# Kernel tuning notes

Measured on AMD Instinct MI355X. Metric: run time of the kernel, lower is better.

## Reference

```python
import jax, jax.numpy as jnp
import numpy as np

EMB = 1024
HEADS = 16
HEAD_DIM = EMB // HEADS


def setup_inputs() -> dict:
    key = jax.random.key(0)
    ks = jax.random.split(key, 9)
    s = 1.0 / np.sqrt(EMB)
    x = jax.random.normal(ks[0], (2, 2048, EMB), dtype=jnp.float32)
    Wq = jax.random.normal(ks[1], (EMB, EMB), dtype=jnp.float32) * s
    bq = jnp.zeros((EMB,), dtype=jnp.float32)
    Wk = jax.random.normal(ks[2], (EMB, EMB), dtype=jnp.float32) * s
    bk = jnp.zeros((EMB,), dtype=jnp.float32)
    Wv = jax.random.normal(ks[3], (EMB, EMB), dtype=jnp.float32) * s
    bv = jnp.zeros((EMB,), dtype=jnp.float32)
    Wo = jax.random.normal(ks[4], (EMB, EMB), dtype=jnp.float32) * s
    bo = jnp.zeros((EMB,), dtype=jnp.float32)
    return {"x": x, "Wq": Wq, "bq": bq, "Wk": Wk, "bk": bk,
            "Wv": Wv, "bv": bv, "Wo": Wo, "bo": bo}


def reference(x, Wq, bq, Wk, bk, Wv, bv, Wo, bo):
    B, S, E = x.shape
    # torch Linear: y = x @ W.T + b
    q = x @ Wq.T + bq
    k = x @ Wk.T + bk
    v = x @ Wv.T + bv
    # [B,S,E] -> [B,H,S,D]
    q = q.reshape(B, S, HEADS, HEAD_DIM).transpose(0, 2, 1, 3)
    k = k.reshape(B, S, HEADS, HEAD_DIM).transpose(0, 2, 1, 3)
    v = v.reshape(B, S, HEADS, HEAD_DIM).transpose(0, 2, 1, 3)
    energy = jnp.einsum('bhqd,bhkd->bhqk', q, k)
    scaling = jnp.float32(E) ** 0.5  # NOTE: sqrt(emb_size), not sqrt(head_dim), as in source
    att = jax.nn.softmax(energy / scaling, axis=-1)
    out = jnp.einsum('bhqk,bhkd->bhqd', att, v)
    out = out.transpose(0, 2, 1, 3).reshape(B, S, E)
    return out @ Wo.T + bo
```

## Files before the change

kernel.cpp:

```cpp
#include <hip/hip_runtime.h>
#include <stdint.h>


typedef _Float16 half8  __attribute__((ext_vector_type(8)));
typedef _Float16 half4v __attribute__((ext_vector_type(4)));
typedef _Float16 half2v __attribute__((ext_vector_type(2)));
typedef float    f32x4  __attribute__((ext_vector_type(4)));

#define GLD16(g, l) __builtin_amdgcn_global_load_lds(                         \
    (__attribute__((address_space(1))) void*)(g),                            \
    (__attribute__((address_space(3))) void*)(l), 16, 0, 0)

#define MFMA16(a, b, c) __builtin_amdgcn_mfma_f32_16x16x32_f16((a), (b), (c), 0, 0, 0)

#if __has_builtin(__builtin_amdgcn_exp2f)
#define EXP2(x) __builtin_amdgcn_exp2f(x)
#else
#define EXP2(x) exp2f(x)
#endif

static __device__ inline half2v pk_f16(float a, float b)
{
#if __has_builtin(__builtin_amdgcn_cvt_pkrtz)
    auto t = __builtin_amdgcn_cvt_pkrtz(a, b);
    return *(half2v*)&t;
#else
    half2v r = { (_Float16)a, (_Float16)b };
    return r;
#endif
}

__global__ void cvt_all(const float* __restrict__ x,  const float* __restrict__ wq,
                        const float* __restrict__ wk, const float* __restrict__ wv,
                        const float* __restrict__ wo, _Float16* __restrict__ xb,
                        _Float16* __restrict__ wqkv, _Float16* __restrict__ wob)
{
    int i = blockIdx.x * blockDim.x + threadIdx.x;
    const float* src; _Float16* dst; int off;
    if (i < 1048576)      { src = x;  dst = xb;                 off = i; }
    else if (i < 1310720) { src = wq; dst = wqkv;               off = i - 1048576; }
    else if (i < 1572864) { src = wk; dst = wqkv + 1048576;     off = i - 1310720; }
    else if (i < 1835008) { src = wv; dst = wqkv + 2097152;     off = i - 1572864; }
    else                  { src = wo; dst = wob;                off = i - 1835008; }
    float4 f = ((const float4*)src)[off];
    half4v h = { (_Float16)f.x, (_Float16)f.y, (_Float16)f.z, (_Float16)f.w };
    ((half4v*)dst)[off] = h;
}

template<int BN, int MODE>
__global__ __launch_bounds__(256, MODE == 0 ? 3 : 2)
void gemm_f16(const _Float16* __restrict__ A, const _Float16* __restrict__ W,
              const float* __restrict__ b0, const float* __restrict__ b1,
              const float* __restrict__ b2, _Float16* __restrict__ o0,
              _Float16* __restrict__ o1, _Float16* __restrict__ o2,
              float* __restrict__ outf, float qscale)
{
    constexpr int NI = BN / 32;
    __shared__ _Float16 lA[128 * 64];
    __shared__ _Float16 lB[BN * 64];
    const int m0 = blockIdx.y * 128, n0 = blockIdx.x * BN;
    const int tid = threadIdx.x, lane = tid & 63, w = tid >> 6;
    const int wr = (w >> 1) * 64, wc = (w & 1) * (BN / 2);
    const int lrow = lane & 15, lk4 = lane >> 4;
    f32x4 acc[4][NI] = {};

    for (int k0 = 0; k0 < 1024; k0 += 64) {
        __syncthreads();
#pragma unroll
        for (int c = 0; c < 4; ++c) {
            int sidx = c * 256 + tid;
            int row = sidx >> 3, sl = sidx & 7;
            int gc = k0 + ((sl ^ (row & 7)) << 3);
            GLD16(A + (size_t)(m0 + row) * 1024 + gc, lA + (size_t)(c * 256 + w * 64) * 8);
        }
#pragma unroll
        for (int c = 0; c < BN / 32; ++c) {
            int sidx = c * 256 + tid;
            int row = sidx >> 3, sl = sidx & 7;
            int gc = k0 + ((sl ^ (row & 7)) << 3);
            GLD16(W + (size_t)(n0 + row) * 1024 + gc, lB + (size_t)(c * 256 + w * 64) * 8);
        }
        __syncthreads();

#pragma unroll
        for (int kd = 0; kd < 2; ++kd) {
            half8 af[4], bf[NI];
#pragma unroll
            for (int mi = 0; mi < 4; ++mi) {
                int ra = wr + mi * 16 + lrow;
                af[mi] = *(const half8*)(lA + ra * 64 + (((kd * 4 + lk4) ^ (ra & 7)) * 8));
            }
#pragma unroll
            for (int ni = 0; ni < NI; ++ni) {
                int rb = wc + ni * 16 + lrow;
                bf[ni] = *(const half8*)(lB + rb * 64 + (((kd * 4 + lk4) ^ (rb & 7)) * 8));
            }
#pragma unroll
            for (int mi = 0; mi < 4; ++mi)
#pragma unroll
                for (int ni = 0; ni < NI; ++ni)
                    acc[mi][ni] = MFMA16(af[mi], bf[ni], acc[mi][ni]);
        }
    }

    if (MODE == 0) {
        const int which = n0 >> 10;
        const float* bp = which == 0 ? b0 : which == 1 ? b1 : b2;
        _Float16* outh  = which == 0 ? o0 : which == 1 ? o1 : o2;
        const float scale = which == 0 ? qscale : 1.f;
        const int nh = n0 & 1023;
        float bcol[NI];
#pragma unroll
        for (int ni = 0; ni < NI; ++ni) bcol[ni] = bp[nh + wc + ni * 16 + lrow];
#pragma unroll
        for (int mi = 0; mi < 4; ++mi)
#pragma unroll
            for (int ni = 0; ni < NI; ++ni)
#pragma unroll
                for (int r = 0; r < 4; ++r) {
                    int rg = m0 + wr + mi * 16 + lk4 * 4 + r;
                    int cg = nh + wc + ni * 16 + lrow;
                    float v = (acc[mi][ni][r] + bcol[ni]) * scale;
                    int b = rg >> 11, s = rg & 2047, h = cg >> 6, d = cg & 63;
                    outh[(((size_t)b * 16 + h) * 2048 + s) * 64 + d] = (_Float16)v;
                }
    } else {
        float bcol[NI];
#pragma unroll
        for (int ni = 0; ni < NI; ++ni) bcol[ni] = b0[n0 + wc + ni * 16 + lrow];
#pragma unroll
        for (int mi = 0; mi < 4; ++mi)
#pragma unroll
            for (int ni = 0; ni < NI; ++ni)
#pragma unroll
                for (int r = 0; r < 4; ++r) {
                    int rg = m0 + wr + mi * 16 + lk4 * 4 + r;
                    int cg = n0 + wc + ni * 16 + lrow;
                    outf[(size_t)rg * 1024 + cg] = acc[mi][ni][r] + bcol[ni];
                }
    }
}

__global__ __launch_bounds__(256)
void transpose_v(const _Float16* __restrict__ v, _Float16* __restrict__ vt)
{
    __shared__ _Float16 t[64][68];
    const int bh = blockIdx.y, s0 = blockIdx.x * 64;
    const _Float16* vh = v + (size_t)bh * 2048 * 64;
    _Float16* vth = vt + (size_t)bh * 64 * 2048;
    const int tid = threadIdx.x;
#pragma unroll
    for (int j = 0; j < 2; ++j) {
        int ch = j * 256 + tid, r = ch >> 3, c = (ch & 7) * 8;
        half8 d = *(const half8*)(vh + (size_t)(s0 + r) * 64 + c);
#pragma unroll
        for (int i = 0; i < 8; ++i) t[r][c + i] = d[i];
    }
    __syncthreads();
#pragma unroll
    for (int j = 0; j < 2; ++j) {
        int ch = j * 256 + tid, d = ch >> 3, sc = (ch & 7) * 8;
        half8 o;
#pragma unroll
        for (int i = 0; i < 8; ++i) o[i] = t[sc + i][d];
        *(half8*)(vth + (size_t)d * 2048 + s0 + sc) = o;
    }
}

#define KVB 64
#define NT  32
__global__ __launch_bounds__(256, 3)
void attn(const _Float16* __restrict__ q, const _Float16* __restrict__ k,
          const _Float16* __restrict__ vt, _Float16* __restrict__ ao)
{
    __shared__ _Float16 lK[2][KVB * 64];
    __shared__ _Float16 lV[2][64 * KVB];
    __shared__ _Float16 lP[4][32 * KVB];
    const int bid0 = blockIdx.x;
    const int bid = (bid0 & 7) * 64 + (bid0 >> 3);
    const int bh = bid >> 4, q0 = (bid & 15) * 128;
    const int b = bh >> 4, h = bh & 15;
    const int tid = threadIdx.x, lane = tid & 63, w = tid >> 6;
    const int lrow = lane & 15, lk4 = lane >> 4;
    const _Float16* qh = q + (size_t)bh * 2048 * 64;
    const _Float16* kh = k + (size_t)bh * 2048 * 64;
    const _Float16* vth = vt + (size_t)bh * 64 * 2048;

    half8 qf[2][2];
#pragma unroll
    for (int ni = 0; ni < 2; ++ni)
#pragma unroll
        for (int kd = 0; kd < 2; ++kd)
            qf[ni][kd] = *(const half8*)(qh + (size_t)(q0 + w * 32 + ni * 16 + lrow) * 64
                                            + kd * 32 + lk4 * 8);

    float l_[2] = { 0.f, 0.f };
    f32x4 o[2][4] = {};

    auto STAGE = [&](int t, int bs) {
        const int s0 = t * KVB;
#pragma unroll
        for (int c = 0; c < 2; ++c) {
            int sidx = c * 256 + tid;
            int row = sidx >> 3, sl = sidx & 7;
            GLD16(kh + (size_t)(s0 + row) * 64 + ((sl ^ (row & 7)) * 8),
                  lK[bs] + (size_t)(c * 256 + w * 64) * 8);
            GLD16(vth + (size_t)row * 2048 + s0 + ((sl ^ (row & 7)) * 8),
                  lV[bs] + (size_t)(c * 256 + w * 64) * 8);
        }
    };

    STAGE(0, 0);
    STAGE(1, 1);

#pragma unroll 2
    for (int t = 0; t < NT; ++t) {
        const int cur = t & 1;
        if (t < NT - 1) asm volatile("s_waitcnt vmcnt(4)" ::: "memory");
        else            asm volatile("s_waitcnt vmcnt(0)" ::: "memory");
        __builtin_amdgcn_s_barrier();
        __builtin_amdgcn_sched_barrier(0);

        f32x4 e[4][2] = {};
        __builtin_amdgcn_s_setprio(1);
#pragma unroll
        for (int kd = 0; kd < 2; ++kd)
#pragma unroll
            for (int mi = 0; mi < 4; ++mi) {
                int rk = mi * 16 + lrow;
                half8 kf = *(const half8*)(lK[cur] + rk * 64
                                           + (((kd * 4 + lk4) ^ (rk & 7)) * 8));
                e[mi][0] = MFMA16(kf, qf[0][kd], e[mi][0]);
                e[mi][1] = MFMA16(kf, qf[1][kd], e[mi][1]);
            }
        __builtin_amdgcn_s_setprio(0);

#pragma unroll
        for (int mi = 0; mi < 4; ++mi)
#pragma unroll
            for (int ni = 0; ni < 2; ++ni) {
                float p0 = EXP2(e[mi][ni][0]);
                float p1 = EXP2(e[mi][ni][1]);
                float p2 = EXP2(e[mi][ni][2]);
                float p3 = EXP2(e[mi][ni][3]);
                l_[ni] += (p0 + p1) + (p2 + p3);
                half2v lo = pk_f16(p0, p1), hi = pk_f16(p2, p3);
                half4v pb = { lo[0], lo[1], hi[0], hi[1] };
                int qrow = ni * 16 + lrow;
                int slot = (mi * 2 + (lk4 >> 1)) ^ (lrow & 7);
                *(half4v*)(lP[w] + qrow * 64 + slot * 8 + (lk4 & 1) * 4) = pb;
            }

        __builtin_amdgcn_s_setprio(1);
#pragma unroll
        for (int ks = 0; ks < 2; ++ks) {
            half8 pa[2];
#pragma unroll
            for (int miq = 0; miq < 2; ++miq) {
                int qrow = miq * 16 + lrow;
                int slot = (ks * 4 + lk4) ^ (lrow & 7);
                pa[miq] = *(const half8*)(lP[w] + qrow * 64 + slot * 8);
            }
#pragma unroll
            for (int nd = 0; nd < 4; ++nd) {
                int drow = nd * 16 + lrow;
                int slot = (ks * 4 + lk4) ^ (drow & 7);
                half8 vf = *(const half8*)(lV[cur] + drow * 64 + slot * 8);
                o[0][nd] = MFMA16(pa[0], vf, o[0][nd]);
                o[1][nd] = MFMA16(pa[1], vf, o[1][nd]);
            }
        }
        __builtin_amdgcn_s_setprio(0);

        __builtin_amdgcn_s_barrier();
        if (t + 2 < NT) STAGE(t + 2, cur);
    }

#pragma unroll
    for (int ni = 0; ni < 2; ++ni) {
        l_[ni] += __shfl_xor(l_[ni], 16);
        l_[ni] += __shfl_xor(l_[ni], 32);
    }
    float linv[2][4];
#pragma unroll
    for (int r = 0; r < 4; ++r) {
        int qloc = lk4 * 4 + r;
        linv[0][r] = 1.f / __shfl(l_[0], qloc);
        linv[1][r] = 1.f / __shfl(l_[1], qloc);
    }
#pragma unroll
    for (int miq = 0; miq < 2; ++miq)
#pragma unroll
        for (int nd = 0; nd < 4; ++nd)
#pragma unroll
            for (int r = 0; r < 4; ++r) {
                int sg = q0 + w * 32 + miq * 16 + lk4 * 4 + r;
                int d = nd * 16 + lrow;
                float val = o[miq][nd][r] * linv[miq][r];
                ao[((size_t)b * 2048 + sg) * 1024 + h * 64 + d] = (_Float16)val;
            }
}

extern "C" void kernel_launch(void* const* d_in, const int* in_sizes, int n_in,
                              void* d_out, int out_size, void* d_ws, size_t ws_size,
                              hipStream_t stream)
{
    const float* x  = (const float*)d_in[0];
    const float* Wq = (const float*)d_in[1];
    const float* bq = (const float*)d_in[2];
    const float* Wk = (const float*)d_in[3];
    const float* bk = (const float*)d_in[4];
    const float* Wv = (const float*)d_in[5];
    const float* bv = (const float*)d_in[6];
    const float* Wo = (const float*)d_in[7];
    const float* bo = (const float*)d_in[8];
    float* out = (float*)d_out;

    char* ws = (char*)d_ws;
    _Float16* xb   = (_Float16*)(ws);
    _Float16* vtb  = (_Float16*)(ws);
    _Float16* wqkv = (_Float16*)(ws + (8u  << 20));
    _Float16* wob  = (_Float16*)(ws + (14u << 20));
    _Float16* qb   = (_Float16*)(ws + (16u << 20));
    _Float16* kb   = (_Float16*)(ws + (24u << 20));
    _Float16* vb   = (_Float16*)(ws + (32u << 20));
    _Float16* aob  = vb;

    cvt_all<<<8192, 256, 0, stream>>>(x, Wq, Wk, Wv, Wo, xb, wqkv, wob);

    const float qscale = 1.4426950408889634f / 32.f;
    gemm_f16<128, 0><<<dim3(24, 32), 256, 0, stream>>>(
        xb, wqkv, bq, bk, bv, qb, kb, vb, nullptr, qscale);

    transpose_v<<<dim3(32, 32), 256, 0, stream>>>(vb, vtb);

    attn<<<512, 256, 0, stream>>>(qb, kb, vtb, aob);

    gemm_f16<64, 1><<<dim3(16, 32), 256, 0, stream>>>(
        aob, wob, bo, nullptr, nullptr, nullptr, nullptr, nullptr, out, 1.f);
}
```

Baseline: 116.7 us.

## Halve attention query tile to 64 rows and double grid size

The attention kernel now gives each block 64 query rows (16 per wave) instead of 128, launches 1024 blocks instead of 512, and raises the launch-bounds occupancy hint from 3 to 4. The P scratch buffer in shared memory shrinks to match. The aim is more blocks and waves per CU to hide latency and fill the GPU better. The cost is that each K/V tile staged into shared memory is reused by half as many query rows, so K/V global traffic doubles and there are fewer MFMAs per shared-memory load.

```diff
diff --git a/kernel.cpp b/kernel.cpp
--- a/kernel.cpp
+++ b/kernel.cpp
@@ -169,16 +169,16 @@
 
 #define KVB 64
 #define NT  32
-__global__ __launch_bounds__(256, 3)
+__global__ __launch_bounds__(256, 4)
 void attn(const _Float16* __restrict__ q, const _Float16* __restrict__ k,
           const _Float16* __restrict__ vt, _Float16* __restrict__ ao)
 {
     __shared__ _Float16 lK[2][KVB * 64];
     __shared__ _Float16 lV[2][64 * KVB];
-    __shared__ _Float16 lP[4][32 * KVB];
+    __shared__ _Float16 lP[4][16 * KVB];
     const int bid0 = blockIdx.x;
-    const int bid = (bid0 & 7) * 64 + (bid0 >> 3);
-    const int bh = bid >> 4, q0 = (bid & 15) * 128;
+    const int bid = (bid0 & 7) * 128 + (bid0 >> 3);
+    const int bh = bid >> 5, q0 = (bid & 31) * 64;
     const int b = bh >> 4, h = bh & 15;
     const int tid = threadIdx.x, lane = tid & 63, w = tid >> 6;
     const int lrow = lane & 15, lk4 = lane >> 4;
@@ -186,16 +186,14 @@
     const _Float16* kh = k + (size_t)bh * 2048 * 64;
     const _Float16* vth = vt + (size_t)bh * 64 * 2048;
 
-    half8 qf[2][2];
-#pragma unroll
-    for (int ni = 0; ni < 2; ++ni)
-#pragma unroll
-        for (int kd = 0; kd < 2; ++kd)
-            qf[ni][kd] = *(const half8*)(qh + (size_t)(q0 + w * 32 + ni * 16 + lrow) * 64
-                                            + kd * 32 + lk4 * 8);
-
-    float l_[2] = { 0.f, 0.f };
-    f32x4 o[2][4] = {};
+    half8 qf[2];
+#pragma unroll
+    for (int kd = 0; kd < 2; ++kd)
+        qf[kd] = *(const half8*)(qh + (size_t)(q0 + w * 16 + lrow) * 64
+                                    + kd * 32 + lk4 * 8);
+
+    float l_ = 0.f;
+    f32x4 o[4] = {};
 
     auto STAGE = [&](int t, int bs) {
         const int s0 = t * KVB;
@@ -221,7 +219,7 @@
         __builtin_amdgcn_s_barrier();
         __builtin_amdgcn_sched_barrier(0);
 
-        f32x4 e[4][2] = {};
+        f32x4 e[4] = {};
         __builtin_amdgcn_s_setprio(1);
 #pragma unroll
         for (int kd = 0; kd < 2; ++kd)
@@ -230,44 +228,34 @@
                 int rk = mi * 16 + lrow;
                 half8 kf = *(const half8*)(lK[cur] + rk * 64
                                            + (((kd * 4 + lk4) ^ (rk & 7)) * 8));
-                e[mi][0] = MFMA16(kf, qf[0][kd], e[mi][0]);
-                e[mi][1] = MFMA16(kf, qf[1][kd], e[mi][1]);
+                e[mi] = MFMA16(kf, qf[kd], e[mi]);
             }
         __builtin_amdgcn_s_setprio(0);
 
 #pragma unroll
-        for (int mi = 0; mi < 4; ++mi)
-#pragma unroll
-            for (int ni = 0; ni < 2; ++ni) {
-                float p0 = EXP2(e[mi][ni][0]);
-                float p1 = EXP2(e[mi][ni][1]);
-                float p2 = EXP2(e[mi][ni][2]);
-                float p3 = EXP2(e[mi][ni][3]);
-                l_[ni] += (p0 + p1) + (p2 + p3);
-                half2v lo = pk_f16(p0, p1), hi = pk_f16(p2, p3);
-                half4v pb = { lo[0], lo[1], hi[0], hi[1] };
-                int qrow = ni * 16 + lrow;
-                int slot = (mi * 2 + (lk4 >> 1)) ^ (lrow & 7);
-                *(half4v*)(lP[w] + qrow * 64 + slot * 8 + (lk4 & 1) * 4) = pb;
-            }
+        for (int mi = 0; mi < 4; ++mi) {
+            float p0 = EXP2(e[mi][0]);
+            float p1 = EXP2(e[mi][1]);
+            float p2 = EXP2(e[mi][2]);
+            float p3 = EXP2(e[mi][3]);
+            l_ += (p0 + p1) + (p2 + p3);
+            half2v lo = pk_f16(p0, p1), hi = pk_f16(p2, p3);
+            half4v pb = { lo[0], lo[1], hi[0], hi[1] };
+            int slot = (mi * 2 + (lk4 >> 1)) ^ (lrow & 7);
+            *(half4v*)(lP[w] + lrow * 64 + slot * 8 + (lk4 & 1) * 4) = pb;
+        }
 
         __builtin_amdgcn_s_setprio(1);
 #pragma unroll
         for (int ks = 0; ks < 2; ++ks) {
-            half8 pa[2];
-#pragma unroll
-            for (int miq = 0; miq < 2; ++miq) {
-                int qrow = miq * 16 + lrow;
-                int slot = (ks * 4 + lk4) ^ (lrow & 7);
-                pa[miq] = *(const half8*)(lP[w] + qrow * 64 + slot * 8);
-            }
+            int slotp = (ks * 4 + lk4) ^ (lrow & 7);
+            half8 pa = *(const half8*)(lP[w] + lrow * 64 + slotp * 8);
 #pragma unroll
             for (int nd = 0; nd < 4; ++nd) {
                 int drow = nd * 16 + lrow;
                 int slot = (ks * 4 + lk4) ^ (drow & 7);
                 half8 vf = *(const half8*)(lV[cur] + drow * 64 + slot * 8);
-                o[0][nd] = MFMA16(pa[0], vf, o[0][nd]);
-                o[1][nd] = MFMA16(pa[1], vf, o[1][nd]);
+                o[nd] = MFMA16(pa, vf, o[nd]);
             }
         }
         __builtin_amdgcn_s_setprio(0);
@@ -276,29 +264,21 @@
         if (t + 2 < NT) STAGE(t + 2, cur);
     }
 
-#pragma unroll
-    for (int ni = 0; ni < 2; ++ni) {
-        l_[ni] += __shfl_xor(l_[ni], 16);
-        l_[ni] += __shfl_xor(l_[ni], 32);
-    }
-    float linv[2][4];
-#pragma unroll
-    for (int r = 0; r < 4; ++r) {
-        int qloc = lk4 * 4 + r;
-        linv[0][r] = 1.f / __shfl(l_[0], qloc);
-        linv[1][r] = 1.f / __shfl(l_[1], qloc);
-    }
-#pragma unroll
-    for (int miq = 0; miq < 2; ++miq)
-#pragma unroll
-        for (int nd = 0; nd < 4; ++nd)
-#pragma unroll
-            for (int r = 0; r < 4; ++r) {
-                int sg = q0 + w * 32 + miq * 16 + lk4 * 4 + r;
-                int d = nd * 16 + lrow;
-                float val = o[miq][nd][r] * linv[miq][r];
-                ao[((size_t)b * 2048 + sg) * 1024 + h * 64 + d] = (_Float16)val;
-            }
+    l_ += __shfl_xor(l_, 16);
+    l_ += __shfl_xor(l_, 32);
+    float linv[4];
+#pragma unroll
+    for (int r = 0; r < 4; ++r)
+        linv[r] = 1.f / __shfl(l_, lk4 * 4 + r);
+#pragma unroll
+    for (int nd = 0; nd < 4; ++nd)
+#pragma unroll
+        for (int r = 0; r < 4; ++r) {
+            int sg = q0 + w * 16 + lk4 * 4 + r;
+            int d = nd * 16 + lrow;
+            float val = o[nd][r] * linv[r];
+            ao[((size_t)b * 2048 + sg) * 1024 + h * 64 + d] = (_Float16)val;
+        }
 }
 
 extern "C" void kernel_launch(void* const* d_in, const int* in_sizes, int n_in,
@@ -334,7 +314,7 @@
 
     transpose_v<<<dim3(32, 32), 256, 0, stream>>>(vb, vtb);
 
-    attn<<<512, 256, 0, stream>>>(qb, kb, vtb, aob);
+    attn<<<1024, 256, 0, stream>>>(qb, kb, vtb, aob);
 
     gemm_f16<64, 1><<<dim3(16, 32), 256, 0, stream>>>(
         aob, wob, bo, nullptr, nullptr, nullptr, nullptr, nullptr, out, 1.f);
```

Result: no change. 119.0 us (+1.9%).
